# Optimization experiments

Measured on AMD Instinct MI355X. Metric: run time of the kernel, lower is better.

Reference implementation:

```python
import jax, jax.numpy as jnp
import numpy as np

N = 256          # waveguide_dims
ITERN = 3        # iter_num
B = 8192         # batch
INDEX_END = 10   # MNIST classes
ALPHA = 0.1
G = 0.05 * np.pi
PHI_B = np.pi


def setup_inputs() -> dict:
    key = jax.random.key(0)
    k1, k2, k3, k4, k5 = jax.random.split(key, 5)
    two_pi = 2.0 * np.pi
    return {
        "x_real": jax.random.normal(k1, (B, N), dtype=jnp.float32),
        "x_imag": jax.random.normal(k2, (B, N), dtype=jnp.float32),
        "theta": jax.random.uniform(k3, (ITERN, N, N // 2), dtype=jnp.float32) * two_pi,
        "phi":   jax.random.uniform(k4, (ITERN, N, N // 2), dtype=jnp.float32) * two_pi,
        "gamma": jax.random.uniform(k5, (ITERN, N), dtype=jnp.float32) * two_pi,
    }


def _mzi_mesh(x, theta, phi, gamma):
    """Rectangular (Clements) MZI mesh: N layers of 2x2 rotations + output phases.
    x: [B, N] complex64; theta, phi: [N, N//2]; gamma: [N]."""
    L = theta.shape[0]
    shifts = jnp.arange(L) % 2                      # even/odd layer offset
    full = jnp.ones((N // 2,), dtype=bool)
    odd = full.at[-1].set(False)                    # wrap-around pair inactive on odd layers
    masks = jnp.where((shifts == 1)[:, None], odd[None, :], full[None, :])

    def step(xc, inp):
        th, ph, sh, mk = inp
        xr = jnp.roll(xc, -sh, axis=1).reshape(-1, N // 2, 2)
        x0, x1 = xr[..., 0], xr[..., 1]
        half = 0.5 * th
        s, c = jnp.sin(half), jnp.cos(half)
        pre = 1j * jnp.exp(1j * half)               # common MZI prefactor
        ep = jnp.exp(1j * ph)
        y0 = pre * (ep * s * x0 + c * x1)
        y1 = pre * (ep * c * x0 - s * x1)
        y0 = jnp.where(mk, y0, x0)
        y1 = jnp.where(mk, y1, x1)
        y = jnp.stack([y0, y1], axis=-1).reshape(-1, N)
        return jnp.roll(y, sh, axis=1), None

    x, _ = jax.lax.scan(step, x, (theta, phi, shifts, masks))
    return x * jnp.exp(1j * gamma)[None, :]


def _eo_nonlin(x):
    # phase = 0.5*g*|x|^2 + 0.5*phi_b ; out = sqrt(1-alpha)*cos(phase)*exp(-i phase)*x
    phase = 0.5 * G * (x.real ** 2 + x.imag ** 2) + 0.5 * PHI_B
    return np.float32(np.sqrt(1.0 - ALPHA)) * jnp.cos(phase) * jnp.exp(-1j * phase) * x


def reference(x_real, x_imag, theta, phi, gamma):
    x = x_real.astype(jnp.complex64) + 1j * x_imag.astype(jnp.complex64)
    for i in range(ITERN):
        x = _mzi_mesh(x, theta[i], phi[i], gamma[i])
        if i != ITERN - 1:
            x = _eo_nonlin(x)
    intensity = x.real ** 2 + x.imag ** 2            # cnormsq
    norm = jnp.sqrt(jnp.sum(intensity ** 2, axis=1, keepdims=True))
    intensity = intensity / jnp.maximum(norm, 1e-12)  # F.normalize(dim=1)
    return intensity[:, :INDEX_END]
```

## Files before the change

kernel.cpp:

```cpp
#include <hip/hip_runtime.h>
#include <math.h>

#define NWG 256
#define NPAIR 128
#define NITER 3
#define NBATCH 8192
#define KDIM 512
#define MSZ (512*512)

typedef __attribute__((ext_vector_type(8))) short short8;
typedef __attribute__((ext_vector_type(4))) float floatx4;

static __device__ __forceinline__ unsigned short f2bf(float f) {
    unsigned int u = __float_as_uint(f);
    unsigned int r = (u + 0x7fffu + ((u >> 16) & 1u)) >> 16;
    return (unsigned short)r;
}
static __device__ __forceinline__ float bf2f(unsigned short h) {
    return __uint_as_float(((unsigned int)h) << 16);
}
static __device__ __forceinline__ void bsplit(float v, unsigned short &h, unsigned short &l) {
    h = f2bf(v);
    l = f2bf(v - bf2f(h));
}
static __device__ __forceinline__ void async16(const void* g, void* l) {
    __builtin_amdgcn_global_load_lds(
        (const __attribute__((address_space(1))) unsigned int*)g,
        (__attribute__((address_space(3))) unsigned int*)l, 16, 0, 0);
}

static __device__ __forceinline__ void apply2(
    float &x0r, float &x0i, float &x1r, float &x1i,
    const float4 a, const float4 b)
{
    float y0r = a.x*x0r - a.y*x0i + a.z*x1r - a.w*x1i;
    float y0i = a.x*x0i + a.y*x0r + a.z*x1i + a.w*x1r;
    float y1r = b.x*x0r - b.y*x0i + b.z*x1r - b.w*x1i;
    float y1i = b.x*x0i + b.y*x0r + b.z*x1i + b.w*x1r;
    x0r = y0r; x0i = y0i; x1r = y1r; x1i = y1i;
}

__global__ void precompute_kernel(const float* __restrict__ theta,
                                  const float* __restrict__ phi,
                                  const float* __restrict__ gamma,
                                  float* __restrict__ coef,
                                  float* __restrict__ coefT,
                                  float* __restrict__ gexp)
{
    int idx = blockIdx.x * blockDim.x + threadIdx.x;
    if (idx < NITER * NWG * NPAIR) {
        float h  = 0.5f * theta[idx];
        float ph = phi[idx];
        float sh = sinf(h),  ch = cosf(h);
        float sp = sinf(ph), cp = cosf(ph);
        float pr = -sh, pii = ch;
        float qr = pr*cp - pii*sp;
        float qi = pr*sp + pii*cp;
        float Ar = qr*sh,  Ai = qi*sh;
        float Br = pr*ch,  Bi = pii*ch;
        float Cr = qr*ch,  Ci = qi*ch;
        float Dr = -pr*sh, Di = -pii*sh;
        float4* o = (float4*)coef + (size_t)idx * 2;
        o[0] = make_float4(Ar,Ai,Br,Bi);
        o[1] = make_float4(Cr,Ci,Dr,Di);
        float4* ot = (float4*)coefT + (size_t)idx * 2;
        ot[0] = make_float4(Ar,Ai,Cr,Ci);
        ot[1] = make_float4(Br,Bi,Dr,Di);
    }
    if (idx < NITER * NWG) {
        float g = gamma[idx];
        gexp[idx*2]   = cosf(g);
        gexp[idx*2+1] = sinf(g);
    }
}

static __device__ __forceinline__ void store_row(
    unsigned short* __restrict__ bh, unsigned short* __restrict__ bl,
    int row, int lane, bool cj, const float xr[4], const float xi[4])
{
    ushort4 reH, reL, imH, imL, nimH, nimL;
    unsigned short h, l;
#pragma unroll
    for (int e = 0; e < 4; ++e) {
        bsplit(xr[e], h, l);  ((unsigned short*)&reH)[e]  = h; ((unsigned short*)&reL)[e]  = l;
        bsplit(xi[e], h, l);  ((unsigned short*)&imH)[e]  = h; ((unsigned short*)&imL)[e]  = l;
        bsplit(-xi[e], h, l); ((unsigned short*)&nimH)[e] = h; ((unsigned short*)&nimL)[e] = l;
    }
    ushort4 urH = cj ? imH : nimH, urL = cj ? imL : nimL;
    ushort4 llH = cj ? nimH : imH, llL = cj ? nimL : imL;
    *(ushort4*)(bh + (size_t)row*KDIM + 4*lane)             = reH;
    *(ushort4*)(bh + (size_t)row*KDIM + 256 + 4*lane)       = urH;
    *(ushort4*)(bh + (size_t)(row+256)*KDIM + 4*lane)       = llH;
    *(ushort4*)(bh + (size_t)(row+256)*KDIM + 256 + 4*lane) = reH;
    *(ushort4*)(bl + (size_t)row*KDIM + 4*lane)             = reL;
    *(ushort4*)(bl + (size_t)row*KDIM + 256 + 4*lane)       = urL;
    *(ushort4*)(bl + (size_t)(row+256)*KDIM + 4*lane)       = llL;
    *(ushort4*)(bl + (size_t)(row+256)*KDIM + 256 + 4*lane) = reL;
}

static __device__ __forceinline__ void layer_compute(
    const float4 cc[4], int lane, int sp, float xr[4], float xi[4])
{
    const float4 c0a = cc[0], c0b = cc[1], c1a = cc[2], c1b = cc[3];
    if ((sp & 1) == 0) {
        apply2(xr[0], xi[0], xr[1], xi[1], c0a, c0b);
        apply2(xr[2], xi[2], xr[3], xi[3], c1a, c1b);
    } else {
        float tr = __shfl_down(xr[0], 1, 64);
        float ti = __shfl_down(xi[0], 1, 64);
        apply2(xr[1], xi[1], xr[2], xi[2], c0a, c0b);
        float x3r = xr[3], x3i = xi[3];
        float y3r = c1a.x*x3r - c1a.y*x3i + c1a.z*tr - c1a.w*ti;
        float y3i = c1a.x*x3i + c1a.y*x3r + c1a.z*ti + c1a.w*tr;
        float ynr = c1b.x*x3r - c1b.y*x3i + c1b.z*tr - c1b.w*ti;
        float yni = c1b.x*x3i + c1b.y*x3r + c1b.z*ti + c1b.w*tr;
        float rr = __shfl_up(ynr, 1, 64);
        float ri = __shfl_up(yni, 1, 64);
        if (lane != 63) { xr[3] = y3r; xi[3] = y3i; }
        if (lane != 0)  { xr[0] = rr;  xi[0] = ri; }
    }
}

__global__ void propagate_kernel(const float* __restrict__ coef,
                                 const float* __restrict__ coefT,
                                 const float* __restrict__ gexp,
                                 unsigned short* __restrict__ chunkH,
                                 unsigned short* __restrict__ chunkL)
{
    __shared__ __align__(16) char smem[3 * 16384];

    const int tid  = threadIdx.x;
    const int lane = tid & 63;
    const int wv   = tid >> 6;
    const int grp  = blockIdx.x >> 6;
    const int it   = grp >> 2, c = grp & 3;
    const int row  = (blockIdx.x & 63) * 4 + wv;
    const bool rev = (c & 1);
    const bool cj  = (c == 1) || (c == 2);

    float xr[4], xi[4];
    float gc = 1.0f, gs = 0.0f;
    if (c == 3) { gc = gexp[(it*NWG + row)*2]; gs = gexp[(it*NWG + row)*2 + 1]; }
#pragma unroll
    for (int e = 0; e < 4; ++e) {
        bool on = (4*lane + e) == row;
        xr[e] = on ? gc : 0.0f;
        xi[e] = on ? gs : 0.0f;
    }

    const char* cbb = (const char*)(rev ? coefT : coef)
                    + (size_t)(it*NWG + c*64) * (NPAIR * 32);
    const int slot16 = (tid ^ ((tid >> 3) & 3)) * 16;

    auto stage = [&](int m) {
        char* dst = smem + (m % 3) * 16384;
#pragma unroll
        for (int q = 0; q < 4; ++q) {
            int s = 4*m + q;
            int r = rev ? 63 - s : s;
            async16(cbb + (size_t)r * 4096 + slot16, dst + q*4096 + tid * 16);
        }
    };

    stage(0); stage(1);

    const int sw = (lane >> 1) & 3;
    for (int m = 0; m < 16; ++m) {
        if (m < 15) asm volatile("s_waitcnt vmcnt(4)" ::: "memory");
        else        asm volatile("s_waitcnt vmcnt(0)" ::: "memory");
        __builtin_amdgcn_s_barrier();
        asm volatile("" ::: "memory");
        if (m < 14) stage(m + 2);
        const char* B = smem + (m % 3) * 16384;

        float4 cc[4][4];
#pragma unroll
        for (int q = 0; q < 4; ++q) {
            const char* Bq = B + q*4096;
            cc[q][0] = *(const float4*)(Bq + 16*(4*lane + (0 ^ sw)));
            cc[q][1] = *(const float4*)(Bq + 16*(4*lane + (1 ^ sw)));
            cc[q][2] = *(const float4*)(Bq + 16*(4*lane + (2 ^ sw)));
            cc[q][3] = *(const float4*)(Bq + 16*(4*lane + (3 ^ sw)));
        }
#pragma unroll
        for (int q = 0; q < 4; ++q) {
            int s = 4*m + q;
            layer_compute(cc[q], lane, rev ? 63 - s : s, xr, xi);
        }
    }

    unsigned short* bh = chunkH + (size_t)grp * MSZ;
    unsigned short* bl = chunkL + (size_t)grp * MSZ;
    store_row(bh, bl, row, lane, cj, xr, xi);
}

__global__ __launch_bounds__(256, 2) void compose_kernel(
    const unsigned short* __restrict__ srcH, const unsigned short* __restrict__ srcL,
    unsigned short* __restrict__ outH, unsigned short* __restrict__ outL,
    unsigned short* __restrict__ bmat, int mode)
{
    __shared__ unsigned short sAh[2048], sAl[2048], sBh[2048], sBl[2048];
    const int z = blockIdx.z;
    const unsigned short *Ah, *Al, *Bh, *Bl;
    if (mode == 0) {
        int it = z >> 1, wh = z & 1;
        int ai = it*4 + (wh ? 3 : 0), bi = it*4 + (wh ? 2 : 1);
        Ah = srcH + (size_t)ai*MSZ; Al = srcL + (size_t)ai*MSZ;
        Bh = srcH + (size_t)bi*MSZ; Bl = srcL + (size_t)bi*MSZ;
    } else {
        Ah = srcH + (size_t)(2*z+1)*MSZ; Al = srcL + (size_t)(2*z+1)*MSZ;
        Bh = srcH + (size_t)(2*z)*MSZ;   Bl = srcL + (size_t)(2*z)*MSZ;
    }
    const int tid = threadIdx.x, lane = tid & 63, wv = tid >> 6;
    const int quad = lane >> 4, l16 = lane & 15;
    const int m0 = blockIdx.x * 64, n0 = blockIdx.y * 64;
    const unsigned short* src = (wv==0)?Ah:(wv==1)?Al:(wv==2)?Bh:Bl;
    unsigned short* dst = (wv==0)?sAh:(wv==1)?sAl:(wv==2)?sBh:sBl;
    const int r0 = (wv < 2) ? m0 : n0;
    const int trowb = lane >> 2, tcol = (lane & 3) * 8;

    floatx4 acc[4] = {};
    for (int kt = 0; kt < KDIM; kt += 32) {
        __syncthreads();
#pragma unroll
        for (int i = 0; i < 4; ++i)
            async16(src + (size_t)(r0 + i*16 + trowb)*KDIM + kt + tcol,
                    dst + i*512 + lane*8);
        __syncthreads();
        short8 ah = *(const short8*)&sAh[(16*wv + l16)*32 + quad*8];
        short8 al = *(const short8*)&sAl[(16*wv + l16)*32 + quad*8];
#pragma unroll
        for (int ni = 0; ni < 4; ++ni) {
            short8 bh = *(const short8*)&sBh[(16*ni + l16)*32 + quad*8];
            short8 bl = *(const short8*)&sBl[(16*ni + l16)*32 + quad*8];
            acc[ni] = __builtin_amdgcn_mfma_f32_16x16x32_bf16(ah, bh, acc[ni], 0,0,0);
            acc[ni] = __builtin_amdgcn_mfma_f32_16x16x32_bf16(ah, bl, acc[ni], 0,0,0);
            acc[ni] = __builtin_amdgcn_mfma_f32_16x16x32_bf16(al, bh, acc[ni], 0,0,0);
        }
    }
#pragma unroll
    for (int ni = 0; ni < 4; ++ni)
#pragma unroll
        for (int rg = 0; rg < 4; ++rg) {
            int r = m0 + 16*wv + quad*4 + rg;
            int cc = n0 + 16*ni + l16;
            float v = acc[ni][rg];
            if (mode == 0) {
                float vs = (((z & 1) == 0) && ((r >= 256) != (cc >= 256))) ? -v : v;
                unsigned short h, l; bsplit(vs, h, l);
                outH[(size_t)z*MSZ + (size_t)r*KDIM + cc] = h;
                outL[(size_t)z*MSZ + (size_t)r*KDIM + cc] = l;
            } else {
                bmat[(size_t)z*MSZ + (size_t)r*KDIM + cc] = f2bf(v);
            }
        }
}

__global__ void convert_kernel(const float* __restrict__ xre,
                               const float* __restrict__ xim,
                               unsigned short* __restrict__ xb)
{
    int idx = blockIdx.x * 256 + threadIdx.x;
    int b = idx >> 8, j = idx & 255;
    xb[(size_t)b * KDIM + j]       = f2bf(xre[idx]);
    xb[(size_t)b * KDIM + 256 + j] = f2bf(xim[idx]);
}

__global__ __launch_bounds__(256, 2) void gemm_kernel(
    const unsigned short* __restrict__ A, const unsigned short* __restrict__ Bm,
    int mode, unsigned short* __restrict__ xout, float* __restrict__ Iout)
{
    __shared__ unsigned short sA[64*32];
    __shared__ unsigned short sB[128*32];
    const int tid = threadIdx.x, lane = tid & 63, wv = tid >> 6;
    const int quad = lane >> 4, l16 = lane & 15;
    const int m0 = blockIdx.x * 64, n0 = blockIdx.y * 64;
    const int trowb = lane >> 2, tcol = (lane & 3) * 8;

    floatx4 acc[8] = {};
    for (int kt = 0; kt < KDIM; kt += 32) {
        __syncthreads();
        async16(A + (size_t)(m0 + 16*wv + trowb)*KDIM + kt + tcol,
                &sA[wv*512 + lane*8]);
#pragma unroll
        for (int j = 0; j < 2; ++j) {
            int trow = 32*wv + 16*j + trowb;
            int grow = (trow < 64) ? (n0 + trow) : (n0 + trow + 192);
            async16(Bm + (size_t)grow*KDIM + kt + tcol,
                    &sB[(32*wv + 16*j)*32 + lane*8]);
        }
        __syncthreads();
        short8 a = *(const short8*)&sA[(16*wv + l16)*32 + quad*8];
#pragma unroll
        for (int ni = 0; ni < 8; ++ni) {
            short8 b = *(const short8*)&sB[(16*ni + l16)*32 + quad*8];
            acc[ni] = __builtin_amdgcn_mfma_f32_16x16x32_bf16(a, b, acc[ni], 0,0,0);
        }
    }
#pragma unroll
    for (int ni = 0; ni < 4; ++ni)
#pragma unroll
        for (int rg = 0; rg < 4; ++rg) {
            int row = m0 + 16*wv + quad*4 + rg;
            int cc  = n0 + 16*ni + l16;
            float yr = acc[ni][rg], yi = acc[ni+4][rg];
            if (mode == 2) {
                Iout[(size_t)row*256 + cc] = yr*yr + yi*yi;
            } else {
                float I = yr*yr + yi*yi;
                float phase = 0.078539816339744831f * I + 1.5707963267948966f;
                float sp, cp; __sincosf(phase, &sp, &cp);
                float f = 0.94868329805051381f * cp;
                xout[(size_t)row*KDIM + cc]       = f2bf(f*(cp*yr + sp*yi));
                xout[(size_t)row*KDIM + cc + 256] = f2bf(f*(cp*yi - sp*yr));
            }
        }
}

__global__ void final_kernel(const float* __restrict__ Ibuf,
                             float* __restrict__ out)
{
    const int lane = threadIdx.x & 63;
    const int wv   = threadIdx.x >> 6;
    const int row  = blockIdx.x * 4 + wv;
    float4 v = *(const float4*)(Ibuf + (size_t)row * 256 + 4*lane);
    float ss = v.x*v.x + v.y*v.y + v.z*v.z + v.w*v.w;
#pragma unroll
    for (int d = 1; d < 64; d <<= 1) ss += __shfl_xor(ss, d, 64);
    float inv = 1.0f / fmaxf(sqrtf(ss), 1e-12f);
    float* o = out + (size_t)row * 10;
    if (lane == 0)      { o[0]=v.x*inv; o[1]=v.y*inv; o[2]=v.z*inv; o[3]=v.w*inv; }
    else if (lane == 1) { o[4]=v.x*inv; o[5]=v.y*inv; o[6]=v.z*inv; o[7]=v.w*inv; }
    else if (lane == 2) { o[8]=v.x*inv; o[9]=v.y*inv; }
}

extern "C" void kernel_launch(void* const* d_in, const int* in_sizes, int n_in,
                              void* d_out, int out_size, void* d_ws, size_t ws_size,
                              hipStream_t stream)
{
    const float* x_real = (const float*)d_in[0];
    const float* x_imag = (const float*)d_in[1];
    const float* theta  = (const float*)d_in[2];
    const float* phi    = (const float*)d_in[3];
    const float* gamma  = (const float*)d_in[4];

    char* ws = (char*)d_ws;
    float* coef  = (float*)(ws + 0);
    float* coefT = (float*)(ws + 3145728);
    float* gexp  = (float*)(ws + 6291456);
    unsigned short* chunkH = (unsigned short*)(ws + 6297600);
    unsigned short* chunkL = (unsigned short*)(ws + 12589056);
    unsigned short* PH   = (unsigned short*)(ws + 0);
    unsigned short* PL   = (unsigned short*)(ws + 3145728);
    unsigned short* xbuf0 = (unsigned short*)(ws + 6297600);
    unsigned short* xbuf1 = (unsigned short*)(ws + 14686208);
    float* Ibuf = (float*)(ws + 14686208);
    unsigned short* Bmat = (unsigned short*)(ws + 23074816);

    precompute_kernel<<<(NITER*NWG*NPAIR + 255)/256, 256, 0, stream>>>(
        theta, phi, gamma, coef, coefT, gexp);

    propagate_kernel<<<768, 256, 0, stream>>>(coef, coefT, gexp, chunkH, chunkL);

    compose_kernel<<<dim3(8,8,6), 256, 0, stream>>>(chunkH, chunkL, PH, PL, Bmat, 0);
    compose_kernel<<<dim3(8,8,3), 256, 0, stream>>>(PH, PL, PH, PL, Bmat, 1);

    convert_kernel<<<NBATCH*NWG/256, 256, 0, stream>>>(x_real, x_imag, xbuf0);

    gemm_kernel<<<dim3(128,4), 256, 0, stream>>>(xbuf0, Bmat,           0, xbuf1, (float*)nullptr);
    gemm_kernel<<<dim3(128,4), 256, 0, stream>>>(xbuf1, Bmat + MSZ,     1, xbuf0, (float*)nullptr);
    gemm_kernel<<<dim3(128,4), 256, 0, stream>>>(xbuf0, Bmat + 2*MSZ,   2, (unsigned short*)nullptr, Ibuf);

    final_kernel<<<NBATCH/4, 256, 0, stream>>>(Ibuf, (float*)d_out);
}
```

Measured before the change: 177.4 us.

## Triple-buffer LDS loads in compose and gemm kernels, vectorize input conversion

The compose and gemm kernels now use a three-stage LDS ring buffer. Async global-to-LDS loads are issued two k-steps ahead, and waits use explicit vmcnt counts with a single barrier per step instead of two __syncthreads per step. This is meant to overlap memory latency with MFMA work. The convert kernel now processes 8 elements per thread with float4 loads and 16-byte stores. Triple buffering triples the shared memory per block, which may lower occupancy, and correctness depends on the hand-counted vmcnt values matching the issued loads.

```diff
diff --git a/kernel.cpp b/kernel.cpp
--- a/kernel.cpp
+++ b/kernel.cpp
@@ -9,6 +9,7 @@
 #define MSZ (512*512)
 
 typedef __attribute__((ext_vector_type(8))) short short8;
+typedef __attribute__((ext_vector_type(8))) unsigned short ushort8v;
 typedef __attribute__((ext_vector_type(4))) float floatx4;
 
 static __device__ __forceinline__ unsigned short f2bf(float f) {
@@ -199,7 +200,7 @@
     unsigned short* __restrict__ outH, unsigned short* __restrict__ outL,
     unsigned short* __restrict__ bmat, int mode)
 {
-    __shared__ unsigned short sAh[2048], sAl[2048], sBh[2048], sBl[2048];
+    __shared__ unsigned short sAh[3][2048], sAl[3][2048], sBh[3][2048], sBl[3][2048];
     const int z = blockIdx.z;
     const unsigned short *Ah, *Al, *Bh, *Bl;
     if (mode == 0) {
@@ -215,24 +216,37 @@
     const int quad = lane >> 4, l16 = lane & 15;
     const int m0 = blockIdx.x * 64, n0 = blockIdx.y * 64;
     const unsigned short* src = (wv==0)?Ah:(wv==1)?Al:(wv==2)?Bh:Bl;
-    unsigned short* dst = (wv==0)?sAh:(wv==1)?sAl:(wv==2)?sBh:sBl;
+    unsigned short (*dstb)[2048] = (wv==0)?sAh:(wv==1)?sAl:(wv==2)?sBh:sBl;
     const int r0 = (wv < 2) ? m0 : n0;
     const int trowb = lane >> 2, tcol = (lane & 3) * 8;
 
+    const unsigned short* sp[4];
+#pragma unroll
+    for (int i = 0; i < 4; ++i)
+        sp[i] = src + (size_t)(r0 + i*16 + trowb)*KDIM + tcol;
+
+    auto stage = [&](int s) {
+        int kt = s * 32, bs = s % 3;
+#pragma unroll
+        for (int i = 0; i < 4; ++i)
+            async16(sp[i] + kt, &dstb[bs][i*512 + lane*8]);
+    };
+    stage(0); stage(1);
+
     floatx4 acc[4] = {};
-    for (int kt = 0; kt < KDIM; kt += 32) {
-        __syncthreads();
-#pragma unroll
-        for (int i = 0; i < 4; ++i)
-            async16(src + (size_t)(r0 + i*16 + trowb)*KDIM + kt + tcol,
-                    dst + i*512 + lane*8);
-        __syncthreads();
-        short8 ah = *(const short8*)&sAh[(16*wv + l16)*32 + quad*8];
-        short8 al = *(const short8*)&sAl[(16*wv + l16)*32 + quad*8];
+    for (int s = 0; s < 16; ++s) {
+        if (s < 15) asm volatile("s_waitcnt vmcnt(4)" ::: "memory");
+        else        asm volatile("s_waitcnt vmcnt(0)" ::: "memory");
+        __builtin_amdgcn_s_barrier();
+        asm volatile("" ::: "memory");
+        if (s < 14) stage(s + 2);
+        const int bs = s % 3;
+        short8 ah = *(const short8*)&sAh[bs][(16*wv + l16)*32 + quad*8];
+        short8 al = *(const short8*)&sAl[bs][(16*wv + l16)*32 + quad*8];
 #pragma unroll
         for (int ni = 0; ni < 4; ++ni) {
-            short8 bh = *(const short8*)&sBh[(16*ni + l16)*32 + quad*8];
-            short8 bl = *(const short8*)&sBl[(16*ni + l16)*32 + quad*8];
+            short8 bh = *(const short8*)&sBh[bs][(16*ni + l16)*32 + quad*8];
+            short8 bl = *(const short8*)&sBl[bs][(16*ni + l16)*32 + quad*8];
             acc[ni] = __builtin_amdgcn_mfma_f32_16x16x32_bf16(ah, bh, acc[ni], 0,0,0);
             acc[ni] = __builtin_amdgcn_mfma_f32_16x16x32_bf16(ah, bl, acc[ni], 0,0,0);
             acc[ni] = __builtin_amdgcn_mfma_f32_16x16x32_bf16(al, bh, acc[ni], 0,0,0);
@@ -261,39 +275,58 @@
                                unsigned short* __restrict__ xb)
 {
     int idx = blockIdx.x * 256 + threadIdx.x;
-    int b = idx >> 8, j = idx & 255;
-    xb[(size_t)b * KDIM + j]       = f2bf(xre[idx]);
-    xb[(size_t)b * KDIM + 256 + j] = f2bf(xim[idx]);
+    int b = idx >> 5, j = (idx & 31) << 3;
+    const float* rp = xre + (size_t)b * 256 + j;
+    const float* ip = xim + (size_t)b * 256 + j;
+    float4 r0 = *(const float4*)rp, r1 = *(const float4*)(rp + 4);
+    float4 i0 = *(const float4*)ip, i1 = *(const float4*)(ip + 4);
+    ushort8v re, im;
+    re[0]=f2bf(r0.x); re[1]=f2bf(r0.y); re[2]=f2bf(r0.z); re[3]=f2bf(r0.w);
+    re[4]=f2bf(r1.x); re[5]=f2bf(r1.y); re[6]=f2bf(r1.z); re[7]=f2bf(r1.w);
+    im[0]=f2bf(i0.x); im[1]=f2bf(i0.y); im[2]=f2bf(i0.z); im[3]=f2bf(i0.w);
+    im[4]=f2bf(i1.x); im[5]=f2bf(i1.y); im[6]=f2bf(i1.z); im[7]=f2bf(i1.w);
+    *(ushort8v*)(xb + (size_t)b * KDIM + j)       = re;
+    *(ushort8v*)(xb + (size_t)b * KDIM + 256 + j) = im;
 }
 
 __global__ __launch_bounds__(256, 2) void gemm_kernel(
     const unsigned short* __restrict__ A, const unsigned short* __restrict__ Bm,
     int mode, unsigned short* __restrict__ xout, float* __restrict__ Iout)
 {
-    __shared__ unsigned short sA[64*32];
-    __shared__ unsigned short sB[128*32];
+    __shared__ unsigned short sA[3][64*32];
+    __shared__ unsigned short sB[3][128*32];
     const int tid = threadIdx.x, lane = tid & 63, wv = tid >> 6;
     const int quad = lane >> 4, l16 = lane & 15;
     const int m0 = blockIdx.x * 64, n0 = blockIdx.y * 64;
     const int trowb = lane >> 2, tcol = (lane & 3) * 8;
 
+    const unsigned short* srcA = A + (size_t)(m0 + 16*wv + trowb)*KDIM + tcol;
+    int trow0 = 32*wv + trowb,  trow1 = 32*wv + 16 + trowb;
+    int grow0 = (trow0 < 64) ? (n0 + trow0) : (n0 + trow0 + 192);
+    int grow1 = (trow1 < 64) ? (n0 + trow1) : (n0 + trow1 + 192);
+    const unsigned short* srcB0 = Bm + (size_t)grow0*KDIM + tcol;
+    const unsigned short* srcB1 = Bm + (size_t)grow1*KDIM + tcol;
+
+    auto stage = [&](int s) {
+        int kt = s * 32, bs = s % 3;
+        async16(srcA  + kt, &sA[bs][wv*512 + lane*8]);
+        async16(srcB0 + kt, &sB[bs][(32*wv)*32 + lane*8]);
+        async16(srcB1 + kt, &sB[bs][(32*wv + 16)*32 + lane*8]);
+    };
+    stage(0); stage(1);
+
     floatx4 acc[8] = {};
-    for (int kt = 0; kt < KDIM; kt += 32) {
-        __syncthreads();
-        async16(A + (size_t)(m0 + 16*wv + trowb)*KDIM + kt + tcol,
-                &sA[wv*512 + lane*8]);
-#pragma unroll
-        for (int j = 0; j < 2; ++j) {
-            int trow = 32*wv + 16*j + trowb;
-            int grow = (trow < 64) ? (n0 + trow) : (n0 + trow + 192);
-            async16(Bm + (size_t)grow*KDIM + kt + tcol,
-                    &sB[(32*wv + 16*j)*32 + lane*8]);
-        }
-        __syncthreads();
-        short8 a = *(const short8*)&sA[(16*wv + l16)*32 + quad*8];
+    for (int s = 0; s < 16; ++s) {
+        if (s < 15) asm volatile("s_waitcnt vmcnt(3)" ::: "memory");
+        else        asm volatile("s_waitcnt vmcnt(0)" ::: "memory");
+        __builtin_amdgcn_s_barrier();
+        asm volatile("" ::: "memory");
+        if (s < 14) stage(s + 2);
+        const int bs = s % 3;
+        short8 a = *(const short8*)&sA[bs][(16*wv + l16)*32 + quad*8];
 #pragma unroll
         for (int ni = 0; ni < 8; ++ni) {
-            short8 b = *(const short8*)&sB[(16*ni + l16)*32 + quad*8];
+            short8 b = *(const short8*)&sB[bs][(16*ni + l16)*32 + quad*8];
             acc[ni] = __builtin_amdgcn_mfma_f32_16x16x32_bf16(a, b, acc[ni], 0,0,0);
         }
     }
@@ -365,7 +398,7 @@
     compose_kernel<<<dim3(8,8,6), 256, 0, stream>>>(chunkH, chunkL, PH, PL, Bmat, 0);
     compose_kernel<<<dim3(8,8,3), 256, 0, stream>>>(PH, PL, PH, PL, Bmat, 1);
 
-    convert_kernel<<<NBATCH*NWG/256, 256, 0, stream>>>(x_real, x_imag, xbuf0);
+    convert_kernel<<<NBATCH*NWG/8/256, 256, 0, stream>>>(x_real, x_imag, xbuf0);
 
     gemm_kernel<<<dim3(128,4), 256, 0, stream>>>(xbuf0, Bmat,           0, xbuf1, (float*)nullptr);
     gemm_kernel<<<dim3(128,4), 256, 0, stream>>>(xbuf1, Bmat + MSZ,     1, xbuf0, (float*)nullptr);
```

Result: faster. 169.6 us (-4.4%).
